# Performance work log

Measured on AMD Instinct MI355X. Metric: run time of the kernel, lower is better.

The kernel has to match this reference:

```python
import jax, jax.numpy as jnp
import numpy as np

N_NODES = 50000
N_EDGES = 800000
N_IN = 128
N_OPEN = 64
N_OUT = 40
N_LAYER = 4


def setup_inputs() -> dict:
    key = jax.random.key(0)
    ks = jax.random.split(key, 8)
    stdv, stdvp = 0.01, 1e-4
    KN1 = jnp.tile(jnp.eye(N_OPEN, dtype=jnp.float32)[None], (N_LAYER, 1, 1)) \
        + jax.random.uniform(ks[3], (N_LAYER, N_OPEN, N_OPEN), jnp.float32) * stdvp
    return {
        "xn": jax.random.normal(ks[0], (1, N_IN, N_NODES), jnp.float32),
        "K1Nopen": jax.random.normal(ks[1], (N_OPEN, N_IN), jnp.float32) * stdv,
        "KNclose": jax.random.normal(ks[2], (N_OUT, N_OPEN), jnp.float32) * stdv,
        "KN1": KN1,
        "att_src": 0.001 * jnp.ones((N_LAYER, 1, N_OPEN), jnp.float32),
        "att_dst": 0.001 * jnp.ones((N_LAYER, 1, N_OPEN), jnp.float32),
        "omega": jnp.ones((N_LAYER, N_OPEN), jnp.float32),
        "edge_i": jax.random.randint(ks[4], (N_EDGES,), 0, N_NODES, jnp.int32),
        "edge_j": jax.random.randint(ks[5], (N_EDGES,), 0, N_NODES, jnp.int32),
    }


def segment_softmax(logits, seg, num_segments):
    # numerically-stable softmax grouped by destination node (torch_geometric.utils.softmax)
    m = jax.ops.segment_max(logits, seg, num_segments=num_segments)
    e = jnp.exp(logits - m[seg])
    d = jax.ops.segment_sum(e, seg, num_segments=num_segments)
    return e / d[seg]


def reference(xn, K1Nopen, KNclose, KN1, att_src, att_dst, omega, edge_i, edge_j):
    N = xn.shape[-1]
    # gcn_norm(add_self_loops=True): augment edge list with self loops
    loops = jnp.arange(N, dtype=edge_i.dtype)
    I = jnp.concatenate([edge_i, loops])
    J = jnp.concatenate([edge_j, loops])

    # opening layer: 1x1 conv == matmul over channels, then relu
    x = jax.nn.relu(jnp.einsum('oc,bcn->bon', K1Nopen, xn))  # (1, nopen, N)

    for i in range(KN1.shape[0]):
        feat = x[0]  # (C, N), H=1 head
        # per-edge attention logits: a_src . x[:, I] + a_dst . x[:, J]
        a = att_src[i, 0] @ feat[:, I] + att_dst[i, 0] @ feat[:, J]  # (E,)
        a = jax.nn.leaky_relu(a, 0.2)
        W = segment_softmax(a, I, N)  # softmax over incoming edges of each node I
        # neighborNode: weighted gather of source features; neighborEdge: scatter-sum to dst
        msg = W[None, :] * feat[:, J]  # (C, E)
        spatial = jax.ops.segment_sum(msg.T, I, num_segments=N).T[None]  # (1, C, N)
        # omega residual mixing (per-channel)
        x = x - omega[i][None, :, None] * (x - spatial)
        # singleLayer openclose, act=False inside, relu outside
        x = jax.nn.relu(jnp.einsum('oc,bcn->bon', KN1[i], x))

    x = jnp.einsum('oc,bcn->bon', KNclose, x)  # (1, num_output, N)
    out = jax.nn.log_softmax(x[0].T, axis=-1)  # (N, num_output)
    return out
```

## Files before the change

### kernel.cpp

```cpp
#include <hip/hip_runtime.h>

#define NN 50000
#define NE 800000
#define NET 850000
#define NB_SCAN 49
#define OPEN_BLOCKS 782
#define EPB 1087

typedef unsigned int uint;
typedef unsigned short ushort;
typedef __attribute__((ext_vector_type(8))) short short8v;
typedef __attribute__((ext_vector_type(4))) float f32x4;

__device__ __forceinline__ float bcast_lane(float v, int l) {
    return __int_as_float(__builtin_amdgcn_readlane(__float_as_int(v), l));
}
__device__ __forceinline__ float wred_max(float v) {
#pragma unroll
    for (int off = 32; off; off >>= 1) v = fmaxf(v, __shfl_xor(v, off, 64));
    return v;
}
__device__ __forceinline__ float wred_sum(float v) {
#pragma unroll
    for (int off = 32; off; off >>= 1) v += __shfl_xor(v, off, 64);
    return v;
}
__device__ __forceinline__ void wred_max2(float& a, float& b) {
#pragma unroll
    for (int off = 32; off; off >>= 1) {
        float ta = __shfl_xor(a, off, 64);
        float tb = __shfl_xor(b, off, 64);
        a = fmaxf(a, ta);
        b = fmaxf(b, tb);
    }
}
__device__ __forceinline__ void wred_sum2(float& a, float& b) {
#pragma unroll
    for (int off = 32; off; off >>= 1) {
        float ta = __shfl_xor(a, off, 64);
        float tb = __shfl_xor(b, off, 64);
        a += ta;
        b += tb;
    }
}
__device__ __forceinline__ ushort f2bf(float f) {
    uint u = __float_as_uint(f);
    return (ushort)((u + 0x7fffu + ((u >> 16) & 1u)) >> 16);
}
__device__ __forceinline__ float bflo(uint u) { return __uint_as_float(u << 16); }
__device__ __forceinline__ float bfhi(uint u) { return __uint_as_float(u & 0xffff0000u); }
__device__ __forceinline__ float lrelu(float a) { return (a > 0.f) ? a : 0.2f * a; }

__device__ __forceinline__ void acc8_fma(float* acc8, float wgt, uint4 v) {
    acc8[0] = fmaf(wgt, bflo(v.x), acc8[0]);
    acc8[1] = fmaf(wgt, bfhi(v.x), acc8[1]);
    acc8[2] = fmaf(wgt, bflo(v.y), acc8[2]);
    acc8[3] = fmaf(wgt, bfhi(v.y), acc8[3]);
    acc8[4] = fmaf(wgt, bflo(v.z), acc8[4]);
    acc8[5] = fmaf(wgt, bfhi(v.z), acc8[5]);
    acc8[6] = fmaf(wgt, bflo(v.w), acc8[6]);
    acc8[7] = fmaf(wgt, bfhi(v.w), acc8[7]);
}
__device__ __forceinline__ uint4 pack8(const float* v) {
    uint4 p;
    p.x = (uint)f2bf(v[0]) | ((uint)f2bf(v[1]) << 16);
    p.y = (uint)f2bf(v[2]) | ((uint)f2bf(v[3]) << 16);
    p.z = (uint)f2bf(v[4]) | ((uint)f2bf(v[5]) << 16);
    p.w = (uint)f2bf(v[6]) | ((uint)f2bf(v[7]) << 16);
    return p;
}

__device__ void node_aggregate_generic(const ushort* __restrict__ xin,
                                       const float* __restrict__ darr,
                                       const int* __restrict__ csrj,
                                       int rs, int deg, float s_n,
                                       int lane, int c8, float* out8) {
    float acc8[8] = {0.f, 0.f, 0.f, 0.f, 0.f, 0.f, 0.f, 0.f};
    int re = rs + deg;
    float mxd = -1e30f;
    for (int e = rs + lane; e < re; e += 64) mxd = fmaxf(mxd, darr[csrj[e]]);
    mxd = wred_max(mxd);
    float mx = lrelu(s_n + mxd);
    float sm = 0.f;
    for (int e = rs + lane; e < re; e += 64)
        sm += __expf(lrelu(s_n + darr[csrj[e]]) - mx);
    sm = wred_sum(sm);
    float inv = 1.f / sm;
    for (int e = rs; e < re; ++e) {
        int j = csrj[e];
        float w = __expf(lrelu(s_n + darr[j]) - mx);
        uint4 v = *(const uint4*)(xin + (((size_t)j) << 6) + (c8 << 3));
        acc8_fma(acc8, w, v);
    }
#pragma unroll
    for (int q = 0; q < 8; ++q) out8[q] = acc8[q] * inv;
}

__device__ __forceinline__ void dual_aggregate(const ushort* __restrict__ xin,
                                               const float* __restrict__ darr,
                                               const int* __restrict__ csrj,
                                               int r0, int deg0, float sn0, int jl0, float dl0,
                                               int r1, int deg1, float sn1, int jl1, float dl1,
                                               int lane, int g, int c8,
                                               float* o0, float* o1) {
    if (deg0 <= 64 && deg1 <= 64) {
        float m0 = dl0, m1 = dl1;
        wred_max2(m0, m1);
        float mx0 = lrelu(sn0 + m0);
        float mx1 = lrelu(sn1 + m1);
        float w0 = (lane < deg0) ? __expf(lrelu(sn0 + dl0) - mx0) : 0.f;
        float w1 = (lane < deg1) ? __expf(lrelu(sn1 + dl1) - mx1) : 0.f;
        float su0 = w0, su1 = w1;
        wred_sum2(su0, su1);
        float inv0 = 1.f / su0, inv1 = 1.f / su1;

        float acc0[8] = {0.f, 0.f, 0.f, 0.f, 0.f, 0.f, 0.f, 0.f};
        float acc1[8] = {0.f, 0.f, 0.f, 0.f, 0.f, 0.f, 0.f, 0.f};
        int md = min(deg0, deg1);
        int tt = 0;
        for (; tt + 16 <= md; tt += 16) {
            int e0 = tt + g, e1 = tt + 8 + g;
            int   ja = __shfl(jl0, e0); float wa = __shfl(w0, e0);
            int   jb = __shfl(jl0, e1); float wb = __shfl(w0, e1);
            int   jc = __shfl(jl1, e0); float wc = __shfl(w1, e0);
            int   jd = __shfl(jl1, e1); float wd = __shfl(w1, e1);
            uint4 va = *(const uint4*)(xin + (((size_t)ja) << 6) + (c8 << 3));
            uint4 vb = *(const uint4*)(xin + (((size_t)jb) << 6) + (c8 << 3));
            uint4 vc = *(const uint4*)(xin + (((size_t)jc) << 6) + (c8 << 3));
            uint4 vd = *(const uint4*)(xin + (((size_t)jd) << 6) + (c8 << 3));
            acc8_fma(acc0, wa, va);
            acc8_fma(acc0, wb, vb);
            acc8_fma(acc1, wc, vc);
            acc8_fma(acc1, wd, vd);
        }
        for (; tt + 8 <= md; tt += 8) {
            int e = tt + g;
            int   ja = __shfl(jl0, e); float wa = __shfl(w0, e);
            int   jc = __shfl(jl1, e); float wc = __shfl(w1, e);
            uint4 va = *(const uint4*)(xin + (((size_t)ja) << 6) + (c8 << 3));
            uint4 vc = *(const uint4*)(xin + (((size_t)jc) << 6) + (c8 << 3));
            acc8_fma(acc0, wa, va);
            acc8_fma(acc1, wc, vc);
        }
        for (int u = tt; u < deg0; u += 8) {
            int e = u + g;
            bool ok = e < deg0;
            int ec = ok ? e : 0;
            int   j = __shfl(jl0, ec);
            float w = ok ? __shfl(w0, ec) : 0.f;
            uint4 v = *(const uint4*)(xin + (((size_t)j) << 6) + (c8 << 3));
            acc8_fma(acc0, w, v);
        }
        for (int u = tt; u < deg1; u += 8) {
            int e = u + g;
            bool ok = e < deg1;
            int ec = ok ? e : 0;
            int   j = __shfl(jl1, ec);
            float w = ok ? __shfl(w1, ec) : 0.f;
            uint4 v = *(const uint4*)(xin + (((size_t)j) << 6) + (c8 << 3));
            acc8_fma(acc1, w, v);
        }
#pragma unroll
        for (int q = 0; q < 8; ++q) {
            float a = acc0[q], b = acc1[q];
            float ta = __shfl_xor(a, 8, 64),  tb = __shfl_xor(b, 8, 64);
            a += ta; b += tb;
            ta = __shfl_xor(a, 16, 64); tb = __shfl_xor(b, 16, 64);
            a += ta; b += tb;
            ta = __shfl_xor(a, 32, 64); tb = __shfl_xor(b, 32, 64);
            a += ta; b += tb;
            o0[q] = a * inv0;
            o1[q] = b * inv1;
        }
    } else {
        node_aggregate_generic(xin, darr, csrj, r0, deg0, sn0, lane, c8, o0);
        node_aggregate_generic(xin, darr, csrj, r1, deg1, sn1, lane, c8, o1);
    }
}

__global__ void k_count(const int* __restrict__ ei, int* __restrict__ cnt) {
    int e = blockIdx.x * blockDim.x + threadIdx.x;
    if (e < NET) {
        int i = (e < NE) ? ei[e] : (e - NE);
        atomicAdd(&cnt[i], 1);
    }
}

__global__ __launch_bounds__(1024) void k_scan1(const int* __restrict__ cnt,
                                                int* __restrict__ rowptr,
                                                int* __restrict__ bsum) {
    __shared__ int sh[1024];
    int t = threadIdx.x;
    int i = blockIdx.x * 1024 + t;
    int v = (i < NN) ? cnt[i] : 0;
    sh[t] = v;
    __syncthreads();
    for (int off = 1; off < 1024; off <<= 1) {
        int add = (t >= off) ? sh[t - off] : 0;
        __syncthreads();
        sh[t] += add;
        __syncthreads();
    }
    int incl = sh[t];
    if (i < NN) rowptr[i] = incl - v;
    if (t == 1023) bsum[blockIdx.x] = incl;
}

__global__ void k_scan2(const int* __restrict__ bsum, int* __restrict__ boff,
                        int* __restrict__ rowptr) {
    int lane = threadIdx.x;
    int v = (lane < NB_SCAN) ? bsum[lane] : 0;
    int p = v;
#pragma unroll
    for (int off = 1; off < 64; off <<= 1) {
        int nv = __shfl_up(p, off, 64);
        if (lane >= off) p += nv;
    }
    if (lane < NB_SCAN) boff[lane] = p - v;
    if (lane == 63) rowptr[NN] = p;
}

__global__ __launch_bounds__(1024) void k_scan3(int* __restrict__ rowptr,
                                                const int* __restrict__ boff,
                                                int* __restrict__ cursor) {
    int i = blockIdx.x * 1024 + threadIdx.x;
    if (i < NN) {
        int r = rowptr[i] + boff[i >> 10];
        rowptr[i] = r;
        cursor[i] = r;
    }
}

__device__ __forceinline__ void fill_phase(const int* __restrict__ ei,
                                           const int* __restrict__ ej,
                                           int* __restrict__ cursor,
                                           int* __restrict__ csrj,
                                           int bid, int t) {
    int base = bid * EPB;
    int end = base + EPB;
    if (end > NET) end = NET;
    for (int e = base + t; e < end; e += 256) {
        int i, j;
        if (e < NE) { i = ei[e]; j = ej[e]; }
        else        { i = e - NE; j = i; }
        int pos = atomicAdd(&cursor[i], 1);
        csrj[pos] = j;
    }
}

__global__ __launch_bounds__(256) void k_openfill(const float* __restrict__ xn,
                                                  const float* __restrict__ K1,
                                                  const float* __restrict__ att_s,
                                                  const float* __restrict__ att_d,
                                                  ushort* __restrict__ x0,
                                                  float* __restrict__ s0,
                                                  float* __restrict__ d0,
                                                  const int* __restrict__ ei,
                                                  const int* __restrict__ ej,
                                                  int* __restrict__ cursor,
                                                  int* __restrict__ csrj) {
    __shared__ float xs[64][65];
    __shared__ float Kt[64][65];
    int t = threadIdx.x;
    int bid = blockIdx.x;

    bool fill_first = (bid & 1);
    if (fill_first) fill_phase(ei, ej, cursor, csrj, bid, t);

    int n0 = bid * 64;
    int tx = t & 15;
    int ty = t >> 4;
    float acc[4][4] = {};

    for (int half = 0; half < 2; ++half) {
        if (half) __syncthreads();
        for (int idx = t; idx < 4096; idx += 256) {
            int c = idx >> 6, o = idx & 63;
            Kt[c][o] = K1[o * 128 + half * 64 + c];
        }
        if (n0 + 64 <= NN) {
            for (int idx = t; idx < 1024; idx += 256) {
                int c = idx >> 4, l4 = (idx & 15) * 4;
                float4 v = *(const float4*)&xn[(size_t)(half * 64 + c) * NN + n0 + l4];
                *(float4*)&xs[c][l4] = v;
            }
        } else {
            for (int idx = t; idx < 4096; idx += 256) {
                int c = idx >> 6, ln = idx & 63;
                int n = n0 + ln;
                xs[c][ln] = (n < NN) ? xn[(size_t)(half * 64 + c) * NN + n] : 0.f;
            }
        }
        __syncthreads();

        for (int c = 0; c < 64; ++c) {
            float4 xv = *(const float4*)&xs[c][ty * 4];
            float4 kv = *(const float4*)&Kt[c][tx * 4];
            acc[0][0] = fmaf(xv.x, kv.x, acc[0][0]); acc[0][1] = fmaf(xv.x, kv.y, acc[0][1]);
            acc[0][2] = fmaf(xv.x, kv.z, acc[0][2]); acc[0][3] = fmaf(xv.x, kv.w, acc[0][3]);
            acc[1][0] = fmaf(xv.y, kv.x, acc[1][0]); acc[1][1] = fmaf(xv.y, kv.y, acc[1][1]);
            acc[1][2] = fmaf(xv.y, kv.z, acc[1][2]); acc[1][3] = fmaf(xv.y, kv.w, acc[1][3]);
            acc[2][0] = fmaf(xv.z, kv.x, acc[2][0]); acc[2][1] = fmaf(xv.z, kv.y, acc[2][1]);
            acc[2][2] = fmaf(xv.z, kv.z, acc[2][2]); acc[2][3] = fmaf(xv.z, kv.w, acc[2][3]);
            acc[3][0] = fmaf(xv.w, kv.x, acc[3][0]); acc[3][1] = fmaf(xv.w, kv.y, acc[3][1]);
            acc[3][2] = fmaf(xv.w, kv.z, acc[3][2]); acc[3][3] = fmaf(xv.w, kv.w, acc[3][3]);
        }
    }

    float asv[4], adv[4];
#pragma unroll
    for (int j = 0; j < 4; ++j) { asv[j] = att_s[tx * 4 + j]; adv[j] = att_d[tx * 4 + j]; }

#pragma unroll
    for (int i = 0; i < 4; ++i) {
        int n = n0 + ty * 4 + i;
        if (n < NN) {
            float4 r;
            r.x = fmaxf(acc[i][0], 0.f); r.y = fmaxf(acc[i][1], 0.f);
            r.z = fmaxf(acc[i][2], 0.f); r.w = fmaxf(acc[i][3], 0.f);
            float ps = r.x * asv[0] + r.y * asv[1] + r.z * asv[2] + r.w * asv[3];
            float pd = r.x * adv[0] + r.y * adv[1] + r.z * adv[2] + r.w * adv[3];
#pragma unroll
            for (int off = 1; off < 16; off <<= 1) {
                ps += __shfl_xor(ps, off, 64);
                pd += __shfl_xor(pd, off, 64);
            }
            if (tx == 0) { s0[n] = ps; d0[n] = pd; }
            ushort4 h;
            h.x = f2bf(r.x); h.y = f2bf(r.y); h.z = f2bf(r.z); h.w = f2bf(r.w);
            *(ushort4*)&x0[(size_t)n * 64 + tx * 4] = h;
        }
    }

    if (!fill_first) fill_phase(ei, ej, cursor, csrj, bid, t);
}

template <int SD>
__global__ __launch_bounds__(256, 4) void k_layer(const ushort* __restrict__ xin,
                                                  ushort* __restrict__ xout,
                                                  const float* __restrict__ sarr,
                                                  const float* __restrict__ darr,
                                                  float* __restrict__ snext,
                                                  float* __restrict__ dnext,
                                                  const int* __restrict__ rowptr,
                                                  const int* __restrict__ csrj,
                                                  const float* __restrict__ Kl,
                                                  const float* __restrict__ om_l,
                                                  const float* __restrict__ atts_n,
                                                  const float* __restrict__ attd_n) {
    __shared__ ushort Tl[32][72];
    __shared__ ushort Kb[64][72];
    __shared__ float spart[32], dpart[32];

    int t = threadIdx.x;
    int lane = t & 63;
    int wid = t >> 6;
    int g = lane >> 3, c8 = lane & 7;

    for (int u = t; u < 512; u += 256) {
        int row = u >> 3, cb = (u & 7) * 8;
        float4 f0 = *(const float4*)&Kl[row * 64 + cb];
        float4 f1 = *(const float4*)&Kl[row * 64 + cb + 4];
        float v8[8] = {f0.x, f0.y, f0.z, f0.w, f1.x, f1.y, f1.z, f1.w};
        *(uint4*)&Kb[row][cb] = pack8(v8);
    }
    if (SD && t < 32) { spart[t] = 0.f; dpart[t] = 0.f; }

    float om8[8];
    {
        float4 a = *(const float4*)&om_l[c8 * 8];
        float4 b = *(const float4*)&om_l[c8 * 8 + 4];
        om8[0] = a.x; om8[1] = a.y; om8[2] = a.z; om8[3] = a.w;
        om8[4] = b.x; om8[5] = b.y; om8[6] = b.z; om8[7] = b.w;
    }

    int nblk = blockIdx.x * 32;

    for (int rp = 0; rp < 4; ++rp) {
        int n0 = nblk + wid * 8 + rp * 2;
        if (n0 < NN) {
            int r0 = rowptr[n0], r1 = rowptr[n0 + 1], r2 = rowptr[n0 + 2];
            int deg0 = r1 - r0, deg1 = r2 - r1;
            float sn0 = sarr[n0], sn1 = sarr[n0 + 1];
            int   jl0 = (lane < deg0) ? csrj[r0 + lane] : 0;
            int   jl1 = (lane < deg1) ? csrj[r1 + lane] : 0;
            float dl0 = (lane < deg0) ? darr[jl0] : -1e30f;
            float dl1 = (lane < deg1) ? darr[jl1] : -1e30f;
            uint4 xcv0 = *(const uint4*)(xin + (((size_t)n0) << 6) + (c8 << 3));
            uint4 xcv1 = *(const uint4*)(xin + (((size_t)(n0 + 1)) << 6) + (c8 << 3));

            float t0a[8], t1a[8];
            dual_aggregate(xin, darr, csrj, r0, deg0, sn0, jl0, dl0,
                           r1, deg1, sn1, jl1, dl1, lane, g, c8, t0a, t1a);

            float xc;
            xc = bflo(xcv0.x); t0a[0] = xc - om8[0] * (xc - t0a[0]);
            xc = bfhi(xcv0.x); t0a[1] = xc - om8[1] * (xc - t0a[1]);
            xc = bflo(xcv0.y); t0a[2] = xc - om8[2] * (xc - t0a[2]);
            xc = bfhi(xcv0.y); t0a[3] = xc - om8[3] * (xc - t0a[3]);
            xc = bflo(xcv0.z); t0a[4] = xc - om8[4] * (xc - t0a[4]);
            xc = bfhi(xcv0.z); t0a[5] = xc - om8[5] * (xc - t0a[5]);
            xc = bflo(xcv0.w); t0a[6] = xc - om8[6] * (xc - t0a[6]);
            xc = bfhi(xcv0.w); t0a[7] = xc - om8[7] * (xc - t0a[7]);
            xc = bflo(xcv1.x); t1a[0] = xc - om8[0] * (xc - t1a[0]);
            xc = bfhi(xcv1.x); t1a[1] = xc - om8[1] * (xc - t1a[1]);
            xc = bflo(xcv1.y); t1a[2] = xc - om8[2] * (xc - t1a[2]);
            xc = bfhi(xcv1.y); t1a[3] = xc - om8[3] * (xc - t1a[3]);
            xc = bflo(xcv1.z); t1a[4] = xc - om8[4] * (xc - t1a[4]);
            xc = bfhi(xcv1.z); t1a[5] = xc - om8[5] * (xc - t1a[5]);
            xc = bflo(xcv1.w); t1a[6] = xc - om8[6] * (xc - t1a[6]);
            xc = bfhi(xcv1.w); t1a[7] = xc - om8[7] * (xc - t1a[7]);

            int lr = n0 - nblk;
            if (g == 0) {
                *(uint4*)&Tl[lr][c8 * 8] = pack8(t0a);
            } else if (g == 1) {
                *(uint4*)&Tl[lr + 1][c8 * 8] = pack8(t1a);
            }
        }
    }
    __syncthreads();

    {
        int mt = wid >> 1;
        int arow = mt * 16 + (lane & 15);
        int koff = (lane >> 4) * 8;
        short8v a0 = *(const short8v*)&Tl[arow][koff];
        short8v a1 = *(const short8v*)&Tl[arow][32 + koff];
        int col0 = (wid & 1) * 32 + (lane & 15);
        int col1 = col0 + 16;
        short8v b00 = *(const short8v*)&Kb[col0][koff];
        short8v b01 = *(const short8v*)&Kb[col0][32 + koff];
        short8v b10 = *(const short8v*)&Kb[col1][koff];
        short8v b11 = *(const short8v*)&Kb[col1][32 + koff];
        f32x4 acc0 = {0.f, 0.f, 0.f, 0.f};
        f32x4 acc1 = {0.f, 0.f, 0.f, 0.f};
        acc0 = __builtin_amdgcn_mfma_f32_16x16x32_bf16(a0, b00, acc0, 0, 0, 0);
        acc0 = __builtin_amdgcn_mfma_f32_16x16x32_bf16(a1, b01, acc0, 0, 0, 0);
        acc1 = __builtin_amdgcn_mfma_f32_16x16x32_bf16(a0, b10, acc1, 0, 0, 0);
        acc1 = __builtin_amdgcn_mfma_f32_16x16x32_bf16(a1, b11, acc1, 0, 0, 0);

        float as0 = 0.f, ad0 = 0.f, as1 = 0.f, ad1 = 0.f;
        if (SD) {
            as0 = atts_n[col0]; ad0 = attd_n[col0];
            as1 = atts_n[col1]; ad1 = attd_n[col1];
        }

        int rbase = mt * 16 + (lane >> 4) * 4;
#pragma unroll
        for (int i = 0; i < 4; ++i) {
            int row = rbase + i;
            int n = nblk + row;
            bool valid = (n < NN);
            float y0 = fmaxf(acc0[i], 0.f);
            float y1 = fmaxf(acc1[i], 0.f);
            if (valid) {
                xout[(size_t)n * 64 + col0] = f2bf(y0);
                xout[(size_t)n * 64 + col1] = f2bf(y1);
            }
            if (SD) {
                float ps = as0 * y0 + as1 * y1;
                float pd = ad0 * y0 + ad1 * y1;
#pragma unroll
                for (int m = 1; m < 16; m <<= 1) {
                    ps += __shfl_xor(ps, m, 64);
                    pd += __shfl_xor(pd, m, 64);
                }
                if ((lane & 15) == 0 && valid) {
                    atomicAdd(&spart[row], ps);
                    atomicAdd(&dpart[row], pd);
                }
            }
        }
    }

    if (SD) {
        __syncthreads();
        if (t < 32) {
            int n = nblk + t;
            if (n < NN) { snext[n] = spart[t]; dnext[n] = dpart[t]; }
        }
    }
}

__global__ __launch_bounds__(512) void k_close(const ushort* __restrict__ xin,
                                               const float* __restrict__ KNc,
                                               float* __restrict__ out) {
    __shared__ float Kpad[40][65];
    int t = threadIdx.x;
    for (int idx = t; idx < 40 * 64; idx += 512)
        Kpad[idx >> 6][idx & 63] = KNc[idx];
    __syncthreads();

    int lane = t & 63;
    int wid = t >> 6;
    int kr = (lane < 40) ? lane : 0;
    int base = (blockIdx.x * 8 + wid) * 4;

#pragma unroll
    for (int p = 0; p < 2; ++p) {
        int n0 = base + p * 2;
        if (n0 >= NN) break;

        float xv0 = bflo((uint)xin[(size_t)n0 * 64 + lane]);
        float xv1 = bflo((uint)xin[(size_t)(n0 + 1) * 64 + lane]);

        float z0a = 0.f, z0b = 0.f, z1a = 0.f, z1b = 0.f;
#pragma unroll
        for (int c = 0; c < 64; c += 2) {
            float k0 = (lane < 40) ? Kpad[kr][c] : 0.f;
            float k1 = (lane < 40) ? Kpad[kr][c + 1] : 0.f;
            float b0 = bcast_lane(xv0, c), b1 = bcast_lane(xv0, c + 1);
            float c0 = bcast_lane(xv1, c), c1 = bcast_lane(xv1, c + 1);
            z0a = fmaf(k0, b0, z0a);
            z0b = fmaf(k1, b1, z0b);
            z1a = fmaf(k0, c0, z1a);
            z1b = fmaf(k1, c1, z1b);
        }
        float z0 = z0a + z0b;
        float z1 = z1a + z1b;

        float zm0 = (lane < 40) ? z0 : -1e30f;
        float zm1 = (lane < 40) ? z1 : -1e30f;
        wred_max2(zm0, zm1);
        float p0 = (lane < 40) ? __expf(z0 - zm0) : 0.f;
        float p1 = (lane < 40) ? __expf(z1 - zm1) : 0.f;
        wred_sum2(p0, p1);
        if (lane < 40) {
            out[(size_t)n0 * 40 + lane] = z0 - zm0 - logf(p0);
            out[(size_t)(n0 + 1) * 40 + lane] = z1 - zm1 - logf(p1);
        }
    }
}

extern "C" void kernel_launch(void* const* d_in, const int* in_sizes, int n_in,
                              void* d_out, int out_size, void* d_ws, size_t ws_size,
                              hipStream_t stream) {
    const float* xn    = (const float*)d_in[0];
    const float* K1    = (const float*)d_in[1];
    const float* KNc   = (const float*)d_in[2];
    const float* KN1   = (const float*)d_in[3];
    const float* atts  = (const float*)d_in[4];
    const float* attd  = (const float*)d_in[5];
    const float* omega = (const float*)d_in[6];
    const int*   ei    = (const int*)d_in[7];
    const int*   ej    = (const int*)d_in[8];
    float* out = (float*)d_out;

    char* ws = (char*)d_ws;
    size_t off = 0;
    auto alloc = [&](size_t b) -> void* {
        void* p = ws + off;
        off = (off + b + 255) & ~(size_t)255;
        return p;
    };
    ushort* xa    = (ushort*)alloc((size_t)NN * 64 * 2);
    ushort* xb    = (ushort*)alloc((size_t)NN * 64 * 2);
    float* sA     = (float*)alloc((size_t)NN * 4);
    float* dA     = (float*)alloc((size_t)NN * 4);
    float* sB     = (float*)alloc((size_t)NN * 4);
    float* dB     = (float*)alloc((size_t)NN * 4);
    int*   rowptr = (int*)alloc((size_t)(NN + 1) * 4);
    int*   cursor = (int*)alloc((size_t)NN * 4);
    int*   csrj   = (int*)alloc((size_t)NET * 4);
    int*   bsum   = (int*)alloc((size_t)NB_SCAN * 4);
    int*   boff   = (int*)alloc((size_t)NB_SCAN * 4);
    if (off > ws_size) return;

    (void)hipMemsetAsync(cursor, 0, (size_t)NN * 4, stream);
    k_count<<<(NET + 255) / 256, 256, 0, stream>>>(ei, cursor);
    k_scan1<<<NB_SCAN, 1024, 0, stream>>>(cursor, rowptr, bsum);
    k_scan2<<<1, 64, 0, stream>>>(bsum, boff, rowptr);
    k_scan3<<<NB_SCAN, 1024, 0, stream>>>(rowptr, boff, cursor);

    k_openfill<<<OPEN_BLOCKS, 256, 0, stream>>>(xn, K1, atts, attd, xa, sA, dA,
                                                ei, ej, cursor, csrj);

    const int LBLK = (NN + 31) / 32;
    const ushort* xi = xa; ushort* xo = xb;
    const float* si = sA; const float* di = dA;
    float* so = sB; float* dn = dB;
    for (int l = 0; l < 3; ++l) {
        k_layer<1><<<LBLK, 256, 0, stream>>>(xi, xo, si, di, so, dn, rowptr, csrj,
                                             KN1 + (size_t)l * 4096, omega + l * 64,
                                             atts + (size_t)(l + 1) * 64,
                                             attd + (size_t)(l + 1) * 64);
        const ushort* t0 = xi; xi = xo; xo = (ushort*)t0;
        const float* t1 = si; si = so; so = (float*)t1;
        const float* t2 = di; di = dn; dn = (float*)t2;
    }
    k_layer<0><<<LBLK, 256, 0, stream>>>(xi, xo, si, di, so, dn, rowptr, csrj,
                                         KN1 + (size_t)3 * 4096, omega + 3 * 64,
                                         atts, attd);

    k_close<<<(NN + 31) / 32, 512, 0, stream>>>(xo, KNc, out);
}
```

Before: 308.2 us.

## Software-pipeline node-pair loads in layer kernel and batch edge atomics

The layer kernel's per-warp loop over four node pairs is now software-pipelined. Rowptr and source-score values for all eight nodes are loaded once into lanes and broadcast with readlane, and the CSR/neighbor/feature loads for the next pair are issued before the current pair is aggregated. The count and fill kernels each thread several edges, and fill issues all its loads, then all atomics, then all stores, to raise memory-level parallelism. This adds register pressure in the layer kernel, which may lower occupancy.

```diff
diff --git a/kernel.cpp b/kernel.cpp
--- a/kernel.cpp
+++ b/kernel.cpp
@@ -14,6 +14,9 @@
 
 __device__ __forceinline__ float bcast_lane(float v, int l) {
     return __int_as_float(__builtin_amdgcn_readlane(__float_as_int(v), l));
+}
+__device__ __forceinline__ int ibcast(int v, int l) {
+    return __builtin_amdgcn_readlane(v, l);
 }
 __device__ __forceinline__ float wred_max(float v) {
 #pragma unroll
@@ -179,10 +182,14 @@
 }
 
 __global__ void k_count(const int* __restrict__ ei, int* __restrict__ cnt) {
-    int e = blockIdx.x * blockDim.x + threadIdx.x;
-    if (e < NET) {
-        int i = (e < NE) ? ei[e] : (e - NE);
-        atomicAdd(&cnt[i], 1);
+    int base = blockIdx.x * 1024 + threadIdx.x;
+#pragma unroll
+    for (int k = 0; k < 4; ++k) {
+        int e = base + k * 256;
+        if (e < NET) {
+            int i = (e < NE) ? ei[e] : (e - NE);
+            atomicAdd(&cnt[i], 1);
+        }
     }
 }
 
@@ -239,13 +246,25 @@
     int base = bid * EPB;
     int end = base + EPB;
     if (end > NET) end = NET;
-    for (int e = base + t; e < end; e += 256) {
-        int i, j;
-        if (e < NE) { i = ei[e]; j = ej[e]; }
-        else        { i = e - NE; j = i; }
-        int pos = atomicAdd(&cursor[i], 1);
-        csrj[pos] = j;
-    }
+    int e0 = base + t, e1 = e0 + 256, e2 = e0 + 512, e3 = e0 + 768, e4 = e0 + 1024;
+    bool o0 = e0 < end, o1 = e1 < end, o2 = e2 < end, o3 = e3 < end, o4 = e4 < end;
+    int i0 = 0, j0 = 0, i1 = 0, j1 = 0, i2 = 0, j2 = 0, i3 = 0, j3 = 0, i4 = 0, j4 = 0;
+    if (o0) { if (e0 < NE) { i0 = ei[e0]; j0 = ej[e0]; } else { i0 = e0 - NE; j0 = i0; } }
+    if (o1) { if (e1 < NE) { i1 = ei[e1]; j1 = ej[e1]; } else { i1 = e1 - NE; j1 = i1; } }
+    if (o2) { if (e2 < NE) { i2 = ei[e2]; j2 = ej[e2]; } else { i2 = e2 - NE; j2 = i2; } }
+    if (o3) { if (e3 < NE) { i3 = ei[e3]; j3 = ej[e3]; } else { i3 = e3 - NE; j3 = i3; } }
+    if (o4) { if (e4 < NE) { i4 = ei[e4]; j4 = ej[e4]; } else { i4 = e4 - NE; j4 = i4; } }
+    int p0 = 0, p1 = 0, p2 = 0, p3 = 0, p4 = 0;
+    if (o0) p0 = atomicAdd(&cursor[i0], 1);
+    if (o1) p1 = atomicAdd(&cursor[i1], 1);
+    if (o2) p2 = atomicAdd(&cursor[i2], 1);
+    if (o3) p3 = atomicAdd(&cursor[i3], 1);
+    if (o4) p4 = atomicAdd(&cursor[i4], 1);
+    if (o0) csrj[p0] = j0;
+    if (o1) csrj[p1] = j1;
+    if (o2) csrj[p2] = j2;
+    if (o3) csrj[p3] = j3;
+    if (o4) csrj[p4] = j4;
 }
 
 __global__ __launch_bounds__(256) void k_openfill(const float* __restrict__ xn,
@@ -375,49 +394,88 @@
     }
 
     int nblk = blockIdx.x * 32;
-
+    int nw0 = nblk + wid * 8;
+
+    int   rpv = ((lane < 9) && (nw0 + lane <= NN)) ? rowptr[nw0 + lane] : 0;
+    float snv = ((lane < 8) && (nw0 + lane < NN)) ? sarr[nw0 + lane] : 0.f;
+
+    const uint4 zero4 = {0u, 0u, 0u, 0u};
+
+    int   c_r0 = ibcast(rpv, 0), c_r1 = ibcast(rpv, 1), c_r2 = ibcast(rpv, 2);
+    bool  c_v = (nw0 < NN);
+    int   c_deg0 = c_v ? (c_r1 - c_r0) : 0;
+    int   c_deg1 = c_v ? (c_r2 - c_r1) : 0;
+    float c_sn0 = bcast_lane(snv, 0), c_sn1 = bcast_lane(snv, 1);
+    int   c_jl0 = (lane < c_deg0) ? csrj[c_r0 + lane] : 0;
+    int   c_jl1 = (lane < c_deg1) ? csrj[c_r1 + lane] : 0;
+    float c_dl0 = (lane < c_deg0) ? darr[c_jl0] : -1e30f;
+    float c_dl1 = (lane < c_deg1) ? darr[c_jl1] : -1e30f;
+    uint4 c_x0 = c_v ? *(const uint4*)(xin + (((size_t)nw0) << 6) + (c8 << 3)) : zero4;
+    uint4 c_x1 = c_v ? *(const uint4*)(xin + (((size_t)(nw0 + 1)) << 6) + (c8 << 3)) : zero4;
+
+#pragma unroll
     for (int rp = 0; rp < 4; ++rp) {
-        int n0 = nblk + wid * 8 + rp * 2;
-        if (n0 < NN) {
-            int r0 = rowptr[n0], r1 = rowptr[n0 + 1], r2 = rowptr[n0 + 2];
-            int deg0 = r1 - r0, deg1 = r2 - r1;
-            float sn0 = sarr[n0], sn1 = sarr[n0 + 1];
-            int   jl0 = (lane < deg0) ? csrj[r0 + lane] : 0;
-            int   jl1 = (lane < deg1) ? csrj[r1 + lane] : 0;
-            float dl0 = (lane < deg0) ? darr[jl0] : -1e30f;
-            float dl1 = (lane < deg1) ? darr[jl1] : -1e30f;
-            uint4 xcv0 = *(const uint4*)(xin + (((size_t)n0) << 6) + (c8 << 3));
-            uint4 xcv1 = *(const uint4*)(xin + (((size_t)(n0 + 1)) << 6) + (c8 << 3));
-
+        int   nx_r0 = 0, nx_r1 = 0, nx_deg0 = 0, nx_deg1 = 0, nx_jl0 = 0, nx_jl1 = 0;
+        float nx_sn0 = 0.f, nx_sn1 = 0.f, nx_dl0 = -1e30f, nx_dl1 = -1e30f;
+        uint4 nx_x0 = zero4, nx_x1 = zero4;
+        bool  nx_v = false;
+        if (rp < 3) {
+            int nn0 = nw0 + 2 * rp + 2;
+            nx_v = (nn0 < NN);
+            nx_r0 = ibcast(rpv, 2 * rp + 2);
+            nx_r1 = ibcast(rpv, 2 * rp + 3);
+            int nx_r2 = ibcast(rpv, 2 * rp + 4);
+            nx_deg0 = nx_v ? (nx_r1 - nx_r0) : 0;
+            nx_deg1 = nx_v ? (nx_r2 - nx_r1) : 0;
+            nx_sn0 = bcast_lane(snv, 2 * rp + 2);
+            nx_sn1 = bcast_lane(snv, 2 * rp + 3);
+            nx_jl0 = (lane < nx_deg0) ? csrj[nx_r0 + lane] : 0;
+            nx_jl1 = (lane < nx_deg1) ? csrj[nx_r1 + lane] : 0;
+            nx_dl0 = (lane < nx_deg0) ? darr[nx_jl0] : -1e30f;
+            nx_dl1 = (lane < nx_deg1) ? darr[nx_jl1] : -1e30f;
+            if (nx_v) {
+                nx_x0 = *(const uint4*)(xin + (((size_t)nn0) << 6) + (c8 << 3));
+                nx_x1 = *(const uint4*)(xin + (((size_t)(nn0 + 1)) << 6) + (c8 << 3));
+            }
+        }
+
+        if (c_v) {
             float t0a[8], t1a[8];
-            dual_aggregate(xin, darr, csrj, r0, deg0, sn0, jl0, dl0,
-                           r1, deg1, sn1, jl1, dl1, lane, g, c8, t0a, t1a);
+            dual_aggregate(xin, darr, csrj, c_r0, c_deg0, c_sn0, c_jl0, c_dl0,
+                           c_r1, c_deg1, c_sn1, c_jl1, c_dl1, lane, g, c8, t0a, t1a);
 
             float xc;
-            xc = bflo(xcv0.x); t0a[0] = xc - om8[0] * (xc - t0a[0]);
-            xc = bfhi(xcv0.x); t0a[1] = xc - om8[1] * (xc - t0a[1]);
-            xc = bflo(xcv0.y); t0a[2] = xc - om8[2] * (xc - t0a[2]);
-            xc = bfhi(xcv0.y); t0a[3] = xc - om8[3] * (xc - t0a[3]);
-            xc = bflo(xcv0.z); t0a[4] = xc - om8[4] * (xc - t0a[4]);
-            xc = bfhi(xcv0.z); t0a[5] = xc - om8[5] * (xc - t0a[5]);
-            xc = bflo(xcv0.w); t0a[6] = xc - om8[6] * (xc - t0a[6]);
-            xc = bfhi(xcv0.w); t0a[7] = xc - om8[7] * (xc - t0a[7]);
-            xc = bflo(xcv1.x); t1a[0] = xc - om8[0] * (xc - t1a[0]);
-            xc = bfhi(xcv1.x); t1a[1] = xc - om8[1] * (xc - t1a[1]);
-            xc = bflo(xcv1.y); t1a[2] = xc - om8[2] * (xc - t1a[2]);
-            xc = bfhi(xcv1.y); t1a[3] = xc - om8[3] * (xc - t1a[3]);
-            xc = bflo(xcv1.z); t1a[4] = xc - om8[4] * (xc - t1a[4]);
-            xc = bfhi(xcv1.z); t1a[5] = xc - om8[5] * (xc - t1a[5]);
-            xc = bflo(xcv1.w); t1a[6] = xc - om8[6] * (xc - t1a[6]);
-            xc = bfhi(xcv1.w); t1a[7] = xc - om8[7] * (xc - t1a[7]);
-
-            int lr = n0 - nblk;
+            xc = bflo(c_x0.x); t0a[0] = xc - om8[0] * (xc - t0a[0]);
+            xc = bfhi(c_x0.x); t0a[1] = xc - om8[1] * (xc - t0a[1]);
+            xc = bflo(c_x0.y); t0a[2] = xc - om8[2] * (xc - t0a[2]);
+            xc = bfhi(c_x0.y); t0a[3] = xc - om8[3] * (xc - t0a[3]);
+            xc = bflo(c_x0.z); t0a[4] = xc - om8[4] * (xc - t0a[4]);
+            xc = bfhi(c_x0.z); t0a[5] = xc - om8[5] * (xc - t0a[5]);
+            xc = bflo(c_x0.w); t0a[6] = xc - om8[6] * (xc - t0a[6]);
+            xc = bfhi(c_x0.w); t0a[7] = xc - om8[7] * (xc - t0a[7]);
+            xc = bflo(c_x1.x); t1a[0] = xc - om8[0] * (xc - t1a[0]);
+            xc = bfhi(c_x1.x); t1a[1] = xc - om8[1] * (xc - t1a[1]);
+            xc = bflo(c_x1.y); t1a[2] = xc - om8[2] * (xc - t1a[2]);
+            xc = bfhi(c_x1.y); t1a[3] = xc - om8[3] * (xc - t1a[3]);
+            xc = bflo(c_x1.z); t1a[4] = xc - om8[4] * (xc - t1a[4]);
+            xc = bfhi(c_x1.z); t1a[5] = xc - om8[5] * (xc - t1a[5]);
+            xc = bflo(c_x1.w); t1a[6] = xc - om8[6] * (xc - t1a[6]);
+            xc = bfhi(c_x1.w); t1a[7] = xc - om8[7] * (xc - t1a[7]);
+
+            int lr = wid * 8 + 2 * rp;
             if (g == 0) {
                 *(uint4*)&Tl[lr][c8 * 8] = pack8(t0a);
             } else if (g == 1) {
                 *(uint4*)&Tl[lr + 1][c8 * 8] = pack8(t1a);
             }
         }
+
+        c_r0 = nx_r0; c_r1 = nx_r1; c_v = nx_v;
+        c_deg0 = nx_deg0; c_deg1 = nx_deg1;
+        c_sn0 = nx_sn0; c_sn1 = nx_sn1;
+        c_jl0 = nx_jl0; c_jl1 = nx_jl1;
+        c_dl0 = nx_dl0; c_dl1 = nx_dl1;
+        c_x0 = nx_x0; c_x1 = nx_x1;
     }
     __syncthreads();
 
@@ -568,7 +626,7 @@
     if (off > ws_size) return;
 
     (void)hipMemsetAsync(cursor, 0, (size_t)NN * 4, stream);
-    k_count<<<(NET + 255) / 256, 256, 0, stream>>>(ei, cursor);
+    k_count<<<(NET + 1023) / 1024, 256, 0, stream>>>(ei, cursor);
     k_scan1<<<NB_SCAN, 1024, 0, stream>>>(cursor, rowptr, bsum);
     k_scan2<<<1, 64, 0, stream>>>(bsum, boff, rowptr);
     k_scan3<<<NB_SCAN, 1024, 0, stream>>>(rowptr, boff, cursor);
```

After: 308.8 us. Within noise of the previous version (+0.2%).
